# Kernel optimization log

Measured on AMD Instinct MI355X. Metric: run time of the kernel, lower is better.

Reference implementation:

```python
import jax, jax.numpy as jnp
import numpy as np

GROUP_SIZE = 32


def setup_inputs() -> dict:
    key = jax.random.key(0)
    k1, k2 = jax.random.split(key)
    R, L = 4096, 16384
    G = L // GROUP_SIZE  # 512 groups
    weight = jax.random.normal(k1, (R, L), dtype=jnp.float32)
    eps_param = jnp.zeros((G,), dtype=jnp.float32)  # eps_init = 0.0
    adversarial_delta = 0.01 * jax.random.normal(k2, (G,), dtype=jnp.float32)
    return {"weight": weight, "eps_param": eps_param, "adversarial_delta": adversarial_delta}


def reference(weight, eps_param, adversarial_delta):
    L = weight.shape[-1]
    G = L // GROUP_SIZE
    # eps in [-0.5, 0.5], plus adversarial delta, clamped
    eps = 0.5 * jnp.tanh(eps_param)
    eps_eff = jnp.clip(eps + adversarial_delta, -0.5, 0.5)  # [G]

    # group along last dim; shared exponent reduces over ALL leading dims too
    wg = weight.reshape(-1, G, GROUP_SIZE)  # [R, G, gs]
    max_abs = jnp.max(jnp.abs(wg), axis=(0, 2))  # [G]
    e_base = jnp.where(max_abs > 0, jnp.floor(jnp.log2(max_abs)), 0.0)  # [G]
    # in torch, e_base comes from .item() -> constant w.r.t. autograd
    scale = jax.lax.stop_gradient(jnp.exp2(e_base))  # [G]

    s = scale[None, :, None]
    ratio = jnp.clip(jnp.abs(wg) / s, 0.0, 1.0)
    shifted = jnp.clip(ratio + eps_eff[None, :, None], 0.0, 1.0)
    mantissa_q = jnp.round(shifted * 8.0) / 8.0  # 3-bit mantissa grid
    quant = jnp.sign(wg) * s * mantissa_q

    quant_w = quant.reshape(weight.shape)
    return quant_w, jax.lax.stop_gradient(eps_eff), e_base
```

## Files before the change

kernel.cpp:

```cpp
#include <hip/hip_runtime.h>
#include <hip/hip_cooperative_groups.h>
#include <math.h>

namespace cg = cooperative_groups;

#define NROWS 4096
#define NCOLS 16384
#define NGRP  512
#define TOTAL_ELEMS (67108864ULL)
#define TOTAL4      (16777216ULL)
#define GRID_BLOCKS 1024
#define BLOCK 256
#define STRIDE ((size_t)GRID_BLOCKS * BLOCK)

typedef float nfloat4 __attribute__((ext_vector_type(4)));


__global__ void init_kernel(unsigned int* __restrict__ gmax) {
    gmax[threadIdx.x] = 0u;
}

__device__ __forceinline__ float quant1(float a, float s, float inv, float ee) {
    float r  = fminf(fabsf(a) * inv, 1.f);
    float sh = fminf(fmaxf(r + ee, 0.f), 1.f);
    float mq = rintf(sh * 8.f) * 0.125f;
    float q  = copysignf(s * mq, a);
    return (a == 0.f) ? 0.f : q;
}

__global__ void __launch_bounds__(BLOCK, 4)
fused_kernel(const float4* __restrict__ w,
             const float* __restrict__ eps_param,
             const float* __restrict__ delta,
             unsigned int* __restrict__ gmax,
             float* __restrict__ tail,
             float4* __restrict__ out) {
    __shared__ unsigned int smax[NGRP];
    for (int i = threadIdx.x; i < NGRP; i += BLOCK) smax[i] = 0u;
    __syncthreads();

    const size_t tid0 = (size_t)blockIdx.x * BLOCK + threadIdx.x;
    const int g = (int)((tid0 & 4095) >> 3);

    float m0 = 0.f, m1 = 0.f;
    for (size_t i = tid0; i < TOTAL4; i += 2 * STRIDE) {
        float4 a = w[i];
        float4 b = w[i + STRIDE];
        m0 = fmaxf(m0, fmaxf(fmaxf(fabsf(a.x), fabsf(a.y)),
                             fmaxf(fabsf(a.z), fabsf(a.w))));
        m1 = fmaxf(m1, fmaxf(fmaxf(fabsf(b.x), fabsf(b.y)),
                             fmaxf(fabsf(b.z), fabsf(b.w))));
    }
    float m = fmaxf(m0, m1);
    m = fmaxf(m, __shfl_xor(m, 1, 64));
    m = fmaxf(m, __shfl_xor(m, 2, 64));
    m = fmaxf(m, __shfl_xor(m, 4, 64));
    if ((threadIdx.x & 7) == 0)
        atomicMax(&smax[g], __float_as_uint(m));
    __syncthreads();
    for (int j = threadIdx.x; j < NGRP; j += BLOCK)
        if (smax[j]) atomicMax(&gmax[j], smax[j]);

    cg::this_grid().sync();

    unsigned mb = __hip_atomic_load(&gmax[g], __ATOMIC_RELAXED,
                                    __HIP_MEMORY_SCOPE_AGENT);
    float ma = __uint_as_float(mb);
    float e = 0.f;
    if (ma > 0.f) {
        int ex;
        (void)frexpf(ma, &ex);
        e = (float)(ex - 1);
    }
    float eps = 0.5f * tanhf(eps_param[g]);
    float ee  = fminf(fmaxf(eps + delta[g], -0.5f), 0.5f);
    const int   ei  = (int)e;
    const float s   = __uint_as_float((unsigned)(ei + 127) << 23);
    const float inv = __uint_as_float((unsigned)(127 - ei) << 23);

    if (tid0 < 4096 && (tid0 & 7) == 0) {
        tail[g]        = ee;
        tail[NGRP + g] = e;
    }

    for (size_t ii = 0; ii < TOTAL4; ii += 2 * STRIDE) {
        size_t i = (TOTAL4 - 2 * STRIDE - ii) + tid0;
        float4 a = w[i];
        float4 b = w[i + STRIDE];
        nfloat4 oa, ob;
        oa.x = quant1(a.x, s, inv, ee);
        oa.y = quant1(a.y, s, inv, ee);
        oa.z = quant1(a.z, s, inv, ee);
        oa.w = quant1(a.w, s, inv, ee);
        __builtin_nontemporal_store(oa, (nfloat4*)&out[i]);
        ob.x = quant1(b.x, s, inv, ee);
        ob.y = quant1(b.y, s, inv, ee);
        ob.z = quant1(b.z, s, inv, ee);
        ob.w = quant1(b.w, s, inv, ee);
        __builtin_nontemporal_store(ob, (nfloat4*)&out[i + STRIDE]);
    }
}

extern "C" void kernel_launch(void* const* d_in, const int* in_sizes, int n_in,
                              void* d_out, int out_size, void* d_ws, size_t ws_size,
                              hipStream_t stream) {
    const float4* w4       = (const float4*)d_in[0];
    const float* eps_param = (const float*)d_in[1];
    const float* delta     = (const float*)d_in[2];
    float* out  = (float*)d_out;
    float* tail = out + TOTAL_ELEMS;
    unsigned int* gmax = (unsigned int*)d_ws;
    float4* out4 = (float4*)out;

    init_kernel<<<1, NGRP, 0, stream>>>(gmax);

    void* args[] = { (void*)&w4, (void*)&eps_param, (void*)&delta,
                     (void*)&gmax, (void*)&tail, (void*)&out4 };
    hipLaunchCooperativeKernel((const void*)fused_kernel,
                               dim3(GRID_BLOCKS), dim3(BLOCK),
                               args, 0, stream);
}
```

Measured before the change: 574.5 us.

## Double cooperative grid, unroll loads by four, drop shared-memory max staging

Sets the cooperative grid size at runtime from occupancy, using 2048 blocks when they fit, and raises launch bounds to 8 blocks per CU. Both passes now issue four float4 loads per thread per iteration instead of two, giving more memory-level parallelism. The shared-memory per-block max reduction is removed, so each 8-lane leader does a global atomicMax directly. This adds more global atomic traffic and changes register pressure in exchange for more bytes in flight for the bandwidth-bound streaming passes.

```diff
diff --git a/kernel.cpp b/kernel.cpp
--- a/kernel.cpp
+++ b/kernel.cpp
@@ -9,15 +9,17 @@
 #define NGRP  512
 #define TOTAL_ELEMS (67108864ULL)
 #define TOTAL4      (16777216ULL)
-#define GRID_BLOCKS 1024
 #define BLOCK 256
-#define STRIDE ((size_t)GRID_BLOCKS * BLOCK)
 
 typedef float nfloat4 __attribute__((ext_vector_type(4)));
 
 
 __global__ void init_kernel(unsigned int* __restrict__ gmax) {
     gmax[threadIdx.x] = 0u;
+}
+
+__device__ __forceinline__ float absmax4(float4 v) {
+    return fmaxf(fmaxf(fabsf(v.x), fabsf(v.y)), fmaxf(fabsf(v.z), fabsf(v.w)));
 }
 
 __device__ __forceinline__ float quant1(float a, float s, float inv, float ee) {
@@ -28,38 +30,34 @@
     return (a == 0.f) ? 0.f : q;
 }
 
-__global__ void __launch_bounds__(BLOCK, 4)
+__global__ void __launch_bounds__(BLOCK, 8)
 fused_kernel(const float4* __restrict__ w,
              const float* __restrict__ eps_param,
              const float* __restrict__ delta,
              unsigned int* __restrict__ gmax,
              float* __restrict__ tail,
              float4* __restrict__ out) {
-    __shared__ unsigned int smax[NGRP];
-    for (int i = threadIdx.x; i < NGRP; i += BLOCK) smax[i] = 0u;
-    __syncthreads();
-
-    const size_t tid0 = (size_t)blockIdx.x * BLOCK + threadIdx.x;
+    const size_t tid0   = (size_t)blockIdx.x * BLOCK + threadIdx.x;
+    const size_t stride = (size_t)gridDim.x * BLOCK;
     const int g = (int)((tid0 & 4095) >> 3);
 
-    float m0 = 0.f, m1 = 0.f;
-    for (size_t i = tid0; i < TOTAL4; i += 2 * STRIDE) {
+    float m0 = 0.f, m1 = 0.f, m2 = 0.f, m3 = 0.f;
+    for (size_t i = tid0; i < TOTAL4; i += 4 * stride) {
         float4 a = w[i];
-        float4 b = w[i + STRIDE];
-        m0 = fmaxf(m0, fmaxf(fmaxf(fabsf(a.x), fabsf(a.y)),
-                             fmaxf(fabsf(a.z), fabsf(a.w))));
-        m1 = fmaxf(m1, fmaxf(fmaxf(fabsf(b.x), fabsf(b.y)),
-                             fmaxf(fabsf(b.z), fabsf(b.w))));
+        float4 b = w[i + stride];
+        float4 c = w[i + 2 * stride];
+        float4 d = w[i + 3 * stride];
+        m0 = fmaxf(m0, absmax4(a));
+        m1 = fmaxf(m1, absmax4(b));
+        m2 = fmaxf(m2, absmax4(c));
+        m3 = fmaxf(m3, absmax4(d));
     }
-    float m = fmaxf(m0, m1);
+    float m = fmaxf(fmaxf(m0, m1), fmaxf(m2, m3));
     m = fmaxf(m, __shfl_xor(m, 1, 64));
     m = fmaxf(m, __shfl_xor(m, 2, 64));
     m = fmaxf(m, __shfl_xor(m, 4, 64));
     if ((threadIdx.x & 7) == 0)
-        atomicMax(&smax[g], __float_as_uint(m));
-    __syncthreads();
-    for (int j = threadIdx.x; j < NGRP; j += BLOCK)
-        if (smax[j]) atomicMax(&gmax[j], smax[j]);
+        atomicMax(&gmax[g], __float_as_uint(m));
 
     cg::this_grid().sync();
 
@@ -83,21 +81,25 @@
         tail[NGRP + g] = e;
     }
 
-    for (size_t ii = 0; ii < TOTAL4; ii += 2 * STRIDE) {
-        size_t i = (TOTAL4 - 2 * STRIDE - ii) + tid0;
-        float4 a = w[i];
-        float4 b = w[i + STRIDE];
-        nfloat4 oa, ob;
-        oa.x = quant1(a.x, s, inv, ee);
-        oa.y = quant1(a.y, s, inv, ee);
-        oa.z = quant1(a.z, s, inv, ee);
-        oa.w = quant1(a.w, s, inv, ee);
-        __builtin_nontemporal_store(oa, (nfloat4*)&out[i]);
-        ob.x = quant1(b.x, s, inv, ee);
-        ob.y = quant1(b.y, s, inv, ee);
-        ob.z = quant1(b.z, s, inv, ee);
-        ob.w = quant1(b.w, s, inv, ee);
-        __builtin_nontemporal_store(ob, (nfloat4*)&out[i + STRIDE]);
+    for (size_t ii = 4 * stride; ii <= TOTAL4; ii += 4 * stride) {
+        size_t base = (TOTAL4 - ii) + tid0;
+        float4 a = w[base];
+        float4 b = w[base + stride];
+        float4 c = w[base + 2 * stride];
+        float4 d = w[base + 3 * stride];
+        nfloat4 oa, ob, oc, od;
+        oa.x = quant1(a.x, s, inv, ee); oa.y = quant1(a.y, s, inv, ee);
+        oa.z = quant1(a.z, s, inv, ee); oa.w = quant1(a.w, s, inv, ee);
+        __builtin_nontemporal_store(oa, (nfloat4*)&out[base]);
+        ob.x = quant1(b.x, s, inv, ee); ob.y = quant1(b.y, s, inv, ee);
+        ob.z = quant1(b.z, s, inv, ee); ob.w = quant1(b.w, s, inv, ee);
+        __builtin_nontemporal_store(ob, (nfloat4*)&out[base + stride]);
+        oc.x = quant1(c.x, s, inv, ee); oc.y = quant1(c.y, s, inv, ee);
+        oc.z = quant1(c.z, s, inv, ee); oc.w = quant1(c.w, s, inv, ee);
+        __builtin_nontemporal_store(oc, (nfloat4*)&out[base + 2 * stride]);
+        od.x = quant1(d.x, s, inv, ee); od.y = quant1(d.y, s, inv, ee);
+        od.z = quant1(d.z, s, inv, ee); od.w = quant1(d.w, s, inv, ee);
+        __builtin_nontemporal_store(od, (nfloat4*)&out[base + 3 * stride]);
     }
 }
 
@@ -112,11 +114,21 @@
     unsigned int* gmax = (unsigned int*)d_ws;
     float4* out4 = (float4*)out;
 
+    static int nblk = 0;
+    if (nblk == 0) {
+        int occ = 0;
+        hipOccupancyMaxActiveBlocksPerMultiprocessor(&occ, fused_kernel, BLOCK, 0);
+        int ncu = 0;
+        hipDeviceGetAttribute(&ncu, hipDeviceAttributeMultiprocessorCount, 0);
+        if (ncu <= 0) ncu = 256;
+        nblk = (occ * ncu >= 2048) ? 2048 : 1024;
+    }
+
     init_kernel<<<1, NGRP, 0, stream>>>(gmax);
 
     void* args[] = { (void*)&w4, (void*)&eps_param, (void*)&delta,
                      (void*)&gmax, (void*)&tail, (void*)&out4 };
     hipLaunchCooperativeKernel((const void*)fused_kernel,
-                               dim3(GRID_BLOCKS), dim3(BLOCK),
+                               dim3(nblk), dim3(BLOCK),
                                args, 0, stream);
 }
```

After: 597.1 us. +3.9%, slower.
